# Performance work log

Measured on AMD Instinct MI355X. Metric: run time of the kernel, lower is better.

The kernel has to match this reference:

```python
import jax, jax.numpy as jnp
from jax import lax
import numpy as np

B, P, S, K = 16, 4096, 1024, 16   # clouds, points/cloud, fps samples/cloud (ratio 0.25), knn k
IN_F, OUT_F = 256, 512
EPS = 1e-5


def setup_inputs() -> dict:
    key = jax.random.key(0)
    k1, k2, k3 = jax.random.split(key, 3)
    features = jax.random.normal(k1, (B * P, IN_F), jnp.float32)
    positions = jax.random.normal(k2, (B * P, 3), jnp.float32)
    batch = jnp.repeat(jnp.arange(B, dtype=jnp.int32), P)
    W = jax.random.normal(k3, (IN_F, OUT_F), jnp.float32) / np.sqrt(IN_F)
    b = jnp.zeros((OUT_F,), jnp.float32)
    gamma = jnp.ones((OUT_F,), jnp.float32)
    beta = jnp.zeros((OUT_F,), jnp.float32)
    return {"features": features, "positions": positions, "batch": batch,
            "W": W, "b": b, "gamma": gamma, "beta": beta}


def _fps_local(pos):
    """Farthest point sampling on one cloud. pos: [P,3] -> [S] int32 local indices.
    Deterministic start at index 0 (torch_cluster fps with random_start disabled)."""
    def step(carry, _):
        min_d, last = carry
        d = jnp.sum((pos - pos[last]) ** 2, axis=-1)
        min_d = jnp.minimum(min_d, d)
        nxt = jnp.argmax(min_d).astype(jnp.int32)
        return (min_d, nxt), last
    init = (jnp.full((pos.shape[0],), jnp.inf, pos.dtype), jnp.int32(0))
    _, idx = lax.scan(step, init, None, length=S)
    return idx


def _knn_local(q, x):
    """K nearest neighbors of queries q [S,F] among x [P,F] (squared L2). -> [S,K] int32."""
    d = jnp.sum(q * q, -1, keepdims=True) - 2.0 * (q @ x.T) + jnp.sum(x * x, -1)
    _, idx = lax.top_k(-d, K)
    return idx


def reference(features, positions, batch, W, b, gamma, beta):
    pos_b = positions.reshape(B, P, 3)
    feat_b = features.reshape(B, P, IN_F)

    # --- FPS on positions, per cloud ---
    fps_loc = jax.vmap(_fps_local)(pos_b)                      # [B,S]
    offsets = (jnp.arange(B, dtype=jnp.int32) * P)[:, None]    # [B,1]
    fps_glob = (fps_loc + offsets).reshape(-1)                 # [B*S]

    # --- MLP: Linear -> BatchNorm1d (training batch stats, biased var) -> ReLU ---
    h = features @ W + b                                       # [N,OUT_F]
    mu = jnp.mean(h, axis=0)
    var = jnp.var(h, axis=0)
    h = jax.nn.relu(gamma * (h - mu) * lax.rsqrt(var + EPS) + beta)

    # --- brute-force KNN in feature space: queries = features[fps_indices] ---
    q = jnp.take_along_axis(feat_b, fps_loc[..., None], axis=1)   # [B,S,IN_F]
    nn_loc = jax.vmap(_knn_local)(q, feat_b)                      # [B,S,K]
    nn_glob = nn_loc + offsets[..., None]                         # [B,S,K]

    # --- scatter max-pool: each query has exactly K neighbors -> max over K ---
    nb = h[nn_glob.reshape(-1)].reshape(B, S, K, OUT_F)
    new_features = jnp.max(nb, axis=2).reshape(B * S, OUT_F)

    return new_features, positions[fps_glob], batch[fps_glob]
```

## Files before the change

kernel.cpp:

```cpp
#include <hip/hip_runtime.h>
#include <cstddef>


#define TD_B   16
#define TD_P   4096
#define TD_S   1024
#define TD_K   16
#define TD_INF 256
#define TD_OUTF 512

typedef __attribute__((ext_vector_type(8))) _Float16 half8;
typedef __attribute__((ext_vector_type(4))) float    f32x4;
typedef __attribute__((ext_vector_type(2))) float    v2f;

__device__ __forceinline__ unsigned short f2bf(float x) {
    unsigned u = __float_as_uint(x);
    unsigned r = (u + 0x7fffu + ((u >> 16) & 1u)) >> 16;
    return (unsigned short)r;
}

__device__ __forceinline__ int ld_acq(const int* p) {
    return __hip_atomic_load(p, __ATOMIC_ACQUIRE, __HIP_MEMORY_SCOPE_AGENT);
}
__device__ __forceinline__ void st_rel(int* p, int v) {
    __hip_atomic_store(p, v, __ATOMIC_RELEASE, __HIP_MEMORY_SCOPE_AGENT);
}
__device__ __forceinline__ void add_rel(int* p, int v) {
    __hip_atomic_fetch_add(p, v, __ATOMIC_RELEASE, __HIP_MEMORY_SCOPE_AGENT);
}

struct FpsSm {
    float4 p4[TD_P];
    int    sel[TD_S];
    unsigned long long kw[2][4];
};
struct GemmSm {
    float As[16 * 260];
    float Bs[16 * 128];
};
struct KnnSm {
    union {
        _Float16 x[2][32][264];
        float    dt[256][33];
    } u;
    float QQs[256];
    int   QR[256];
    float xxs[32];
};
struct MergeSm {
    float ld[64][130];
    int   li[64][130];
};
struct MaxpSm { int nbr[128]; };
union SmU {
    FpsSm f; GemmSm g; KnnSm k; MergeSm m; MaxpSm mp;
    char pad_[84000];
};

#define TD_DPPSTEPD(kd_, ctl, bc)                                                       \
    {                                                                                   \
        long long ki_ = __double_as_longlong(kd_);                                      \
        unsigned yh_ = (unsigned)__builtin_amdgcn_update_dpp(                           \
            0, (int)((unsigned long long)ki_ >> 32), (ctl), 0xf, 0xf, (bc));            \
        unsigned yl_ = (unsigned)__builtin_amdgcn_update_dpp(                           \
            0, (int)(unsigned)(unsigned long long)ki_, (ctl), 0xf, 0xf, (bc));          \
        kd_ = fmax(kd_, __hiloint2double((int)yh_, (int)yl_));                          \
    }

__global__ __launch_bounds__(512)
void td_all(const float* __restrict__ feat, const float* __restrict__ pos,
            const float* __restrict__ W, const float* __restrict__ bias,
            const float* __restrict__ gamma, const float* __restrict__ beta,
            unsigned short* __restrict__ H, int* __restrict__ FPSI,
            int* __restrict__ NN, float* __restrict__ P1, float* __restrict__ P2,
            float* __restrict__ SS, float* __restrict__ PD, int* __restrict__ PI,
            float* __restrict__ outF, float* __restrict__ outP,
            float* __restrict__ outB, int* __restrict__ flags) {
    __shared__ SmU sm;
    const int bx = blockIdx.x;
    const int t  = threadIdx.x;

    if (bx < 16) {
        __builtin_amdgcn_s_setprio(2);
        const int b = bx;
        const int w = t >> 6;
        v2f px[8], py[8], pz[8], md[8];
        int ni0[8], ni1[8];
        float lx = 0.0f, ly = 0.0f, lz = 0.0f;
        if (t < 256) {
#pragma unroll
            for (int j = 0; j < 8; ++j) {
                int p0 = j * 512 + t, p1 = p0 + 256;
                const float* q0 = pos + (size_t)(b * TD_P + p0) * 3;
                const float* q1 = pos + (size_t)(b * TD_P + p1) * 3;
                float x0 = q0[0], y0 = q0[1], z0 = q0[2];
                float x1 = q1[0], y1 = q1[1], z1 = q1[2];
                px[j] = (v2f){x0, x1}; py[j] = (v2f){y0, y1}; pz[j] = (v2f){z0, z1};
                sm.f.p4[p0] = make_float4(x0, y0, z0, 0.0f);
                sm.f.p4[p1] = make_float4(x1, y1, z1, 0.0f);
                md[j] = (v2f){__builtin_inff(), __builtin_inff()};
                ni0[j] = ~p0; ni1[j] = ~p1;
            }
            if (t == 0) sm.f.sel[0] = 0;
        }
        __syncthreads();
        if (t < 256) { float4 wp = sm.f.p4[0]; lx = wp.x; ly = wp.y; lz = wp.z; }
        for (int s = 0; s < TD_S - 1; ++s) {
            const int par = s & 1;
            if (t < 256) {
                double k[16];
                {
#pragma clang fp contract(off)
                    v2f l2x = (v2f){lx, lx}, l2y = (v2f){ly, ly}, l2z = (v2f){lz, lz};
#pragma unroll
                    for (int j = 0; j < 8; ++j) {
                        v2f dx = px[j] - l2x;
                        v2f dy = py[j] - l2y;
                        v2f dz = pz[j] - l2z;
                        v2f sx = dx * dx;
                        v2f sy = dy * dy;
                        v2f sz = dz * dz;
                        v2f dd = (sx + sy) + sz;
                        md[j] = __builtin_elementwise_min(md[j], dd);
                        k[2 * j]     = __hiloint2double(__float_as_int(md[j].x), ni0[j]);
                        k[2 * j + 1] = __hiloint2double(__float_as_int(md[j].y), ni1[j]);
                    }
                }
#pragma unroll
                for (int st = 8; st > 0; st >>= 1)
#pragma unroll
                    for (int i = 0; i < st; ++i) k[i] = fmax(k[i], k[i + st]);
                double tk = k[0];
                TD_DPPSTEPD(tk, 0x111, true)
                TD_DPPSTEPD(tk, 0x112, true)
                TD_DPPSTEPD(tk, 0x114, true)
                TD_DPPSTEPD(tk, 0x118, true)
                TD_DPPSTEPD(tk, 0x142, false)
                TD_DPPSTEPD(tk, 0x143, false)
                if ((t & 63) == 63)
                    sm.f.kw[par][w] = (unsigned long long)__double_as_longlong(tk);
            }
            __syncthreads();
            if (t < 256) {
                const double2* kd = (const double2*)sm.f.kw[par];
                double2 va = kd[0], vb = kd[1];
                double gk = fmax(fmax(va.x, va.y), fmax(vb.x, vb.y));
                unsigned idx = ~(unsigned)__double2loint(gk);
                if (t == 0) sm.f.sel[s + 1] = (int)idx;
                float4 wp = sm.f.p4[idx];
                lx = wp.x; ly = wp.y; lz = wp.z;
            }
            if (t < 64 && (s & 127) == 127 && s < 896) {
                int c = s >> 7;
                int i0 = c * 128 + 2 * t;
                FPSI[b * TD_S + i0]     = b * TD_P + sm.f.sel[i0];
                FPSI[b * TD_S + i0 + 1] = b * TD_P + sm.f.sel[i0 + 1];
                __threadfence();
                if (t == 0) st_rel(flags + b, c + 1);
            }
        }
        __syncthreads();
        for (int s = t; s < TD_S; s += 512) {
            int li = sm.f.sel[s];
            int og = b * TD_S + s;
            float4 wp = sm.f.p4[li];
            outP[og * 3 + 0] = wp.x;
            outP[og * 3 + 1] = wp.y;
            outP[og * 3 + 2] = wp.z;
            outB[og] = (float)b;
            FPSI[og] = b * TD_P + li;
        }
        __syncthreads();
        if (t == 0) { __threadfence(); st_rel(flags + b, 8); }
    } else if (bx < 16 + 1024) {
        const int gb = bx - 16;
        const int mb = gb >> 2, nb = gb & 3;
        const int tm = t >> 4, tn = t & 15;
        float acc[8][8];
#pragma unroll
        for (int i = 0; i < 8; ++i)
#pragma unroll
            for (int j = 0; j < 8; ++j) acc[i][j] = 0.0f;
        float* As = sm.g.As;
        float* Bs = sm.g.Bs;
        for (int kc = 0; kc < 16; ++kc) {
#pragma unroll
            for (int p2 = 0; p2 < 2; ++p2) {
                int f4 = t + 512 * p2;
                int r = f4 >> 2, c4 = f4 & 3;
                float4 v = *(const float4*)&feat[(size_t)(mb * 256 + r) * 256 + kc * 16 + c4 * 4];
                As[(c4 * 4 + 0) * 260 + r] = v.x;
                As[(c4 * 4 + 1) * 260 + r] = v.y;
                As[(c4 * 4 + 2) * 260 + r] = v.z;
                As[(c4 * 4 + 3) * 260 + r] = v.w;
            }
            {
                int kk = t >> 5, n4 = t & 31;
                float4 v = *(const float4*)&W[(size_t)(kc * 16 + kk) * 512 + nb * 128 + n4 * 4];
                *(float4*)&Bs[kk * 128 + n4 * 4] = v;
            }
            __syncthreads();
#pragma unroll
            for (int kk = 0; kk < 16; ++kk) {
                float4 a0 = *(float4*)&As[kk * 260 + tm * 8];
                float4 a1 = *(float4*)&As[kk * 260 + tm * 8 + 4];
                float4 b0 = *(float4*)&Bs[kk * 128 + tn * 8];
                float4 b1 = *(float4*)&Bs[kk * 128 + tn * 8 + 4];
                float av[8] = {a0.x, a0.y, a0.z, a0.w, a1.x, a1.y, a1.z, a1.w};
                float bv2[8] = {b0.x, b0.y, b0.z, b0.w, b1.x, b1.y, b1.z, b1.w};
#pragma unroll
                for (int i = 0; i < 8; ++i)
#pragma unroll
                    for (int j = 0; j < 8; ++j)
                        acc[i][j] = fmaf(av[i], bv2[j], acc[i][j]);
            }
            __syncthreads();
        }
        float4 bb0 = *(const float4*)&bias[nb * 128 + tn * 8];
        float4 bb1 = *(const float4*)&bias[nb * 128 + tn * 8 + 4];
        float bsv[8] = {bb0.x, bb0.y, bb0.z, bb0.w, bb1.x, bb1.y, bb1.z, bb1.w};
#pragma unroll
        for (int i = 0; i < 8; ++i) {
            int row = mb * 256 + tm * 8 + i;
            uint4 pk;
            pk.x = (unsigned)f2bf(acc[i][0] + bsv[0]) | ((unsigned)f2bf(acc[i][1] + bsv[1]) << 16);
            pk.y = (unsigned)f2bf(acc[i][2] + bsv[2]) | ((unsigned)f2bf(acc[i][3] + bsv[3]) << 16);
            pk.z = (unsigned)f2bf(acc[i][4] + bsv[4]) | ((unsigned)f2bf(acc[i][5] + bsv[5]) << 16);
            pk.w = (unsigned)f2bf(acc[i][6] + bsv[6]) | ((unsigned)f2bf(acc[i][7] + bsv[7]) << 16);
            *(uint4*)&H[(size_t)row * 512 + nb * 128 + tn * 8] = pk;
        }
        __syncthreads();
        if (t == 0) { __threadfence(); add_rel(flags + 16, 1); }
    } else if (bx < 1552) {
        const int kb = bx - 1040;
        const int b = kb & 15, r2 = kb >> 4;
        const int qqp = r2 >> 3, seg = r2 & 7;
        const int segbase = b * TD_P + seg * 512;
        const int qbase = b * TD_S + qqp * 256;
        if (t == 0) {
            while (ld_acq(flags + b) < 2 * qqp + 2) __builtin_amdgcn_s_sleep(16);
        }
        __syncthreads();
        if (t < 256) sm.k.QR[t] = FPSI[qbase + t];
        __syncthreads();

        const int w = t >> 6, lane = t & 63;
        const int m = lane & 15, quad = lane >> 4;

        half8 qh[2][8], ql[2][8];
#pragma unroll
        for (int qs = 0; qs < 2; ++qs) {
            const float* qp = feat + (size_t)sm.k.QR[w * 32 + qs * 16 + m] * 256;
            float qq2 = 0.0f;
#pragma unroll
            for (int ks = 0; ks < 8; ++ks) {
                float4 f0 = *(const float4*)(qp + ks * 32 + quad * 8);
                float4 f1 = *(const float4*)(qp + ks * 32 + quad * 8 + 4);
                float fv[8] = {f0.x, f0.y, f0.z, f0.w, f1.x, f1.y, f1.z, f1.w};
                half8 h, l;
#pragma unroll
                for (int j = 0; j < 8; ++j) {
                    _Float16 hv = (_Float16)fv[j];
                    h[j] = hv;
                    l[j] = (_Float16)(fv[j] - (float)hv);
                    qq2 = fmaf(fv[j], fv[j], qq2);
                }
                qh[qs][ks] = h; ql[qs][ks] = l;
            }
            qq2 += __shfl_xor(qq2, 16, 64);
            qq2 += __shfl_xor(qq2, 32, 64);
            if (quad == 0) sm.k.QQs[w * 32 + qs * 16 + m] = qq2;
        }

        float sd[16]; int si[16];
#pragma unroll
        for (int r = 0; r < 16; ++r) { sd[r] = __builtin_inff(); si[r] = 0x7fffffff; }

        const int xrow = t >> 4, part = t & 15;

        for (int ct = 0; ct < 16; ++ct) {
            __syncthreads();
            {
                const float* xp = feat + (size_t)(segbase + ct * 32 + xrow) * 256 + part * 16;
                float4 f0 = *(const float4*)(xp);
                float4 f1 = *(const float4*)(xp + 4);
                float4 f2 = *(const float4*)(xp + 8);
                float4 f3 = *(const float4*)(xp + 12);
                float fv[16] = {f0.x, f0.y, f0.z, f0.w, f1.x, f1.y, f1.z, f1.w,
                                f2.x, f2.y, f2.z, f2.w, f3.x, f3.y, f3.z, f3.w};
                half8 h0, h1, l0, l1;
                float cn = 0.0f;
#pragma unroll
                for (int j = 0; j < 8; ++j) {
                    _Float16 hv = (_Float16)fv[j];
                    h0[j] = hv; l0[j] = (_Float16)(fv[j] - (float)hv);
                    cn = fmaf(fv[j], fv[j], cn);
                }
#pragma unroll
                for (int j = 0; j < 8; ++j) {
                    float v = fv[8 + j];
                    _Float16 hv = (_Float16)v;
                    h1[j] = hv; l1[j] = (_Float16)(v - (float)hv);
                    cn = fmaf(v, v, cn);
                }
                *(half8*)&sm.k.u.x[0][xrow][part * 16]     = h0;
                *(half8*)&sm.k.u.x[0][xrow][part * 16 + 8] = h1;
                *(half8*)&sm.k.u.x[1][xrow][part * 16]     = l0;
                *(half8*)&sm.k.u.x[1][xrow][part * 16 + 8] = l1;
                cn += __shfl_xor(cn, 1, 64);
                cn += __shfl_xor(cn, 2, 64);
                cn += __shfl_xor(cn, 4, 64);
                cn += __shfl_xor(cn, 8, 64);
                if (part == 0) sm.k.xxs[xrow] = cn;
            }
            __syncthreads();
            f32x4 acc[2][2];
            acc[0][0] = (f32x4)0.0f; acc[0][1] = (f32x4)0.0f;
            acc[1][0] = (f32x4)0.0f; acc[1][1] = (f32x4)0.0f;
#pragma unroll
            for (int ks = 0; ks < 8; ++ks) {
                half8 xh0 = *(half8*)&sm.k.u.x[0][m][ks * 32 + quad * 8];
                half8 xl0 = *(half8*)&sm.k.u.x[1][m][ks * 32 + quad * 8];
                half8 xh1 = *(half8*)&sm.k.u.x[0][16 + m][ks * 32 + quad * 8];
                half8 xl1 = *(half8*)&sm.k.u.x[1][16 + m][ks * 32 + quad * 8];
                acc[0][0] = __builtin_amdgcn_mfma_f32_16x16x32_f16(ql[0][ks], xh0, acc[0][0], 0, 0, 0);
                acc[0][1] = __builtin_amdgcn_mfma_f32_16x16x32_f16(ql[0][ks], xh1, acc[0][1], 0, 0, 0);
                acc[1][0] = __builtin_amdgcn_mfma_f32_16x16x32_f16(ql[1][ks], xh0, acc[1][0], 0, 0, 0);
                acc[1][1] = __builtin_amdgcn_mfma_f32_16x16x32_f16(ql[1][ks], xh1, acc[1][1], 0, 0, 0);
                acc[0][0] = __builtin_amdgcn_mfma_f32_16x16x32_f16(qh[0][ks], xl0, acc[0][0], 0, 0, 0);
                acc[0][1] = __builtin_amdgcn_mfma_f32_16x16x32_f16(qh[0][ks], xl1, acc[0][1], 0, 0, 0);
                acc[1][0] = __builtin_amdgcn_mfma_f32_16x16x32_f16(qh[1][ks], xl0, acc[1][0], 0, 0, 0);
                acc[1][1] = __builtin_amdgcn_mfma_f32_16x16x32_f16(qh[1][ks], xl1, acc[1][1], 0, 0, 0);
                acc[0][0] = __builtin_amdgcn_mfma_f32_16x16x32_f16(qh[0][ks], xh0, acc[0][0], 0, 0, 0);
                acc[0][1] = __builtin_amdgcn_mfma_f32_16x16x32_f16(qh[0][ks], xh1, acc[0][1], 0, 0, 0);
                acc[1][0] = __builtin_amdgcn_mfma_f32_16x16x32_f16(qh[1][ks], xh0, acc[1][0], 0, 0, 0);
                acc[1][1] = __builtin_amdgcn_mfma_f32_16x16x32_f16(qh[1][ks], xh1, acc[1][1], 0, 0, 0);
            }
            __syncthreads();
            {
                float xx0 = sm.k.xxs[m];
                float xx1 = sm.k.xxs[16 + m];
#pragma unroll
                for (int qs = 0; qs < 2; ++qs) {
                    int qb = w * 32 + qs * 16 + quad * 4;
#pragma unroll
                    for (int reg = 0; reg < 4; ++reg) {
                        float qq = sm.k.QQs[qb + reg];
                        sm.k.u.dt[qb + reg][m]      = (qq - 2.0f * acc[qs][0][reg]) + xx0;
                        sm.k.u.dt[qb + reg][16 + m] = (qq - 2.0f * acc[qs][1][reg]) + xx1;
                    }
                }
            }
            __syncthreads();
            if (t < 256) {
                const int ibase = segbase + ct * 32;
                for (int j = 0; j < 32; ++j) {
                    float d = sm.k.u.dt[t][j];
                    if (d < sd[15]) {
                        sd[15] = d; si[15] = ibase + j;
#pragma unroll
                        for (int r = 15; r > 0; --r) {
                            if (sd[r] < sd[r - 1]) {
                                float td2 = sd[r]; sd[r] = sd[r - 1]; sd[r - 1] = td2;
                                int ti = si[r]; si[r] = si[r - 1]; si[r - 1] = ti;
                            }
                        }
                    }
                }
            }
        }
        if (t < 256) {
            size_t o = ((size_t)(qbase + t)) * 128 + seg * 16;
#pragma unroll
            for (int r = 0; r < 16; ++r) { PD[o + r] = sd[r]; PI[o + r] = si[r]; }
        }
        __syncthreads();
        if (t == 0) { __threadfence(); add_rel(flags + 24 + b * 4 + qqp, 1); }
    } else if (bx < 1808) {
        const int rb = bx - 1552;
        if (t == 0) {
            while (ld_acq(flags + 16) < 1024) __builtin_amdgcn_s_sleep(32);
        }
        __syncthreads();
        if (t < 256) {
            float s1a = 0, s2a = 0, s1b = 0, s2b = 0;
            for (int r = 0; r < 256; ++r) {
                const unsigned* hp = (const unsigned*)(H + (size_t)(rb * 256 + r) * 512);
                unsigned u = hp[t];
                float lo = __uint_as_float(u << 16);
                float hi = __uint_as_float(u & 0xffff0000u);
                s1a += lo; s2a = fmaf(lo, lo, s2a);
                s1b += hi; s2b = fmaf(hi, hi, s2b);
            }
            P1[rb * 512 + 2 * t] = s1a; P1[rb * 512 + 2 * t + 1] = s1b;
            P2[rb * 512 + 2 * t] = s2a; P2[rb * 512 + 2 * t + 1] = s2b;
        }
        __syncthreads();
        if (t == 0) { __threadfence(); add_rel(flags + 17, 1); }
    } else if (bx == 1808) {
        if (t == 0) {
            while (ld_acq(flags + 17) < 256) __builtin_amdgcn_s_sleep(32);
        }
        __syncthreads();
        {
            const int ch = t;
            float s1 = 0, s2 = 0;
            for (int rb2 = 0; rb2 < 256; ++rb2) {
                s1 += P1[rb2 * 512 + ch]; s2 += P2[rb2 * 512 + ch];
            }
            const float invN = 1.0f / 65536.0f;
            float mu  = s1 * invN;
            float var = s2 * invN - mu * mu;
            float sc  = gamma[ch] * (1.0f / sqrtf(var + 1e-5f));
            float sh  = beta[ch] - mu * sc;
            SS[ch] = sc; SS[512 + ch] = sh;
        }
        __syncthreads();
        if (t == 0) { __threadfence(); st_rel(flags + 18, 1); }
    } else if (bx < 2065) {
        const int mb = bx - 1809;
        const int cloud = mb >> 4, qqp = (mb >> 2) & 3;
        if (t == 0) {
            while (ld_acq(flags + 24 + cloud * 4 + qqp) < 8) __builtin_amdgcn_s_sleep(16);
        }
        __syncthreads();
        for (int i = t; i < 64 * 128; i += 512) {
            int qi = i >> 7, j = i & 127;
            sm.m.ld[qi][j] = PD[(size_t)mb * 8192 + i];
            sm.m.li[qi][j] = PI[(size_t)mb * 8192 + i];
        }
        __syncthreads();
        if (t < 64) {
            float sd[16]; int si[16];
#pragma unroll
            for (int r = 0; r < 16; ++r) { sd[r] = __builtin_inff(); si[r] = 0x7fffffff; }
            for (int j = 0; j < 128; ++j) {
                float d = sm.m.ld[t][j];
                if (d < sd[15]) {
                    sd[15] = d; si[15] = sm.m.li[t][j];
#pragma unroll
                    for (int r = 15; r > 0; --r) {
                        if (sd[r] < sd[r - 1]) {
                            float td2 = sd[r]; sd[r] = sd[r - 1]; sd[r - 1] = td2;
                            int ti = si[r]; si[r] = si[r - 1]; si[r - 1] = ti;
                        }
                    }
                }
            }
            int og = (mb * 64 + t) * TD_K;
#pragma unroll
            for (int r = 0; r < 16; ++r) NN[og + r] = si[r];
        }
        __syncthreads();
        if (t == 0) { __threadfence(); st_rel(flags + 96 + mb, 1); }
    } else {
        const int pb = bx - 2065;
        const int qbase8 = pb * 8;
        const int mrg = qbase8 >> 6;
        if (t == 0) {
            while (ld_acq(flags + 96 + mrg) == 0) __builtin_amdgcn_s_sleep(16);
            while (ld_acq(flags + 18) == 0) __builtin_amdgcn_s_sleep(16);
        }
        __syncthreads();
        if (t < 128) sm.mp.nbr[t] = NN[(size_t)qbase8 * 16 + t];
        __syncthreads();
        const int hq = t >> 8, tc = t & 255;
        float sc0 = SS[2 * tc], sc1 = SS[2 * tc + 1];
        float sh0 = SS[512 + 2 * tc], sh1 = SS[512 + 2 * tc + 1];
#pragma unroll
        for (int qi = 0; qi < 4; ++qi) {
            const int q = hq * 4 + qi;
            float m0 = 0.0f, m1 = 0.0f;
#pragma unroll
            for (int k = 0; k < 16; ++k) {
                int row = sm.mp.nbr[q * 16 + k];
                unsigned u = ((const unsigned*)(H + (size_t)row * 512))[tc];
                float lo = __uint_as_float(u << 16);
                float hi = __uint_as_float(u & 0xffff0000u);
                m0 = fmaxf(m0, fmaf(sc0, lo, sh0));
                m1 = fmaxf(m1, fmaf(sc1, hi, sh1));
            }
            float2 o; o.x = m0; o.y = m1;
            *(float2*)&outF[(size_t)(qbase8 + q) * 512 + 2 * tc] = o;
        }
    }
}

extern "C" void kernel_launch(void* const* d_in, const int* in_sizes, int n_in,
                              void* d_out, int out_size, void* d_ws, size_t ws_size,
                              hipStream_t stream) {
    const float* feat  = (const float*)d_in[0];
    const float* pos   = (const float*)d_in[1];
    const float* W     = (const float*)d_in[3];
    const float* bias  = (const float*)d_in[4];
    const float* gamma = (const float*)d_in[5];
    const float* beta  = (const float*)d_in[6];

    char* ws = (char*)d_ws;
    int* flags        = (int*)ws;
    unsigned short* H = (unsigned short*)(ws + 4096);
    int*   FPSI = (int*)  (ws + 67112960);
    int*   NN   = (int*)  (ws + 67178496);
    float* P1   = (float*)(ws + 68227072);
    float* P2   = (float*)(ws + 68751360);
    float* SS   = (float*)(ws + 69275648);
    float* PD   = (float*)(ws + 69279744);
    int*   PI   = (int*)  (ws + 77668352);

    float* outF = (float*)d_out;
    float* outP = outF + (size_t)TD_B * TD_S * TD_OUTF;
    float* outB = outP + (size_t)TD_B * TD_S * 3;

    hipMemsetAsync(flags, 0, 2048, stream);
    td_all<<<4113, 512, 0, stream>>>(feat, pos, W, bias, gamma, beta,
                                     H, FPSI, NN, P1, P2, SS, PD, PI,
                                     outF, outP, outB, flags);
}
```

Measured before the change: 1.181 ms.

## Refine KNN granularity to 128-query chunks and reorder persistent block schedule

The KNN blocks now handle 128 queries per chunk instead of 256, so they can start as soon as each eighth of the FPS samples is ready. Merge and maxpool blocks are regrouped per cloud at finer granularity with new flag indices. The BN stats blocks move ahead of the KNN blocks. The last FPS chunk's blocks are placed at the end of the grid. Shared memory padding is dropped and launch bounds request 4 blocks per CU, aiming for higher occupancy and better overlap with the serial FPS. The cost is more blocks, more flag polling, and extra register pressure under the tighter launch bound.

After: 1.683 ms. 1.43x slower.

```diff
diff --git a/kernel.cpp b/kernel.cpp
--- a/kernel.cpp
+++ b/kernel.cpp
@@ -41,20 +41,19 @@
 struct KnnSm {
     union {
         _Float16 x[2][32][264];
-        float    dt[256][33];
+        float    dt[128][33];
     } u;
-    float QQs[256];
-    int   QR[256];
+    float QQs[128];
+    int   QR[128];
     float xxs[32];
 };
 struct MergeSm {
-    float ld[64][130];
-    int   li[64][130];
+    float ld[32][130];
+    int   li[32][130];
 };
 struct MaxpSm { int nbr[128]; };
 union SmU {
     FpsSm f; GemmSm g; KnnSm k; MergeSm m; MaxpSm mp;
-    char pad_[84000];
 };
 
 #define TD_DPPSTEPD(kd_, ctl, bc)                                                       \
@@ -67,7 +66,7 @@
         kd_ = fmax(kd_, __hiloint2double((int)yh_, (int)yl_));                          \
     }
 
-__global__ __launch_bounds__(512)
+__global__ __launch_bounds__(512, 4)
 void td_all(const float* __restrict__ feat, const float* __restrict__ pos,
             const float* __restrict__ W, const float* __restrict__ bias,
             const float* __restrict__ gamma, const float* __restrict__ beta,
@@ -172,7 +171,7 @@
         }
         __syncthreads();
         if (t == 0) { __threadfence(); st_rel(flags + b, 8); }
-    } else if (bx < 16 + 1024) {
+    } else if (bx < 1040) {
         const int gb = bx - 16;
         const int mb = gb >> 2, nb = gb & 3;
         const int tm = t >> 4, tn = t & 15;
@@ -231,26 +230,67 @@
         }
         __syncthreads();
         if (t == 0) { __threadfence(); add_rel(flags + 16, 1); }
-    } else if (bx < 1552) {
-        const int kb = bx - 1040;
-        const int b = kb & 15, r2 = kb >> 4;
-        const int qqp = r2 >> 3, seg = r2 & 7;
+    } else if (bx < 1296) {
+        const int rb = bx - 1040;
+        if (t == 0) {
+            while (ld_acq(flags + 16) < 1024) __builtin_amdgcn_s_sleep(32);
+        }
+        __syncthreads();
+        if (t < 256) {
+            float s1a = 0, s2a = 0, s1b = 0, s2b = 0;
+            for (int r = 0; r < 256; ++r) {
+                const unsigned* hp = (const unsigned*)(H + (size_t)(rb * 256 + r) * 512);
+                unsigned u = hp[t];
+                float lo = __uint_as_float(u << 16);
+                float hi = __uint_as_float(u & 0xffff0000u);
+                s1a += lo; s2a = fmaf(lo, lo, s2a);
+                s1b += hi; s2b = fmaf(hi, hi, s2b);
+            }
+            P1[rb * 512 + 2 * t] = s1a; P1[rb * 512 + 2 * t + 1] = s1b;
+            P2[rb * 512 + 2 * t] = s2a; P2[rb * 512 + 2 * t + 1] = s2b;
+        }
+        __syncthreads();
+        if (t == 0) { __threadfence(); add_rel(flags + 17, 1); }
+    } else if (bx == 1296) {
+        if (t == 0) {
+            while (ld_acq(flags + 17) < 256) __builtin_amdgcn_s_sleep(32);
+        }
+        __syncthreads();
+        {
+            const int ch = t;
+            float s1 = 0, s2 = 0;
+            for (int rb2 = 0; rb2 < 256; ++rb2) {
+                s1 += P1[rb2 * 512 + ch]; s2 += P2[rb2 * 512 + ch];
+            }
+            const float invN = 1.0f / 65536.0f;
+            float mu  = s1 * invN;
+            float var = s2 * invN - mu * mu;
+            float sc  = gamma[ch] * (1.0f / sqrtf(var + 1e-5f));
+            float sh  = beta[ch] - mu * sc;
+            SS[ch] = sc; SS[512 + ch] = sh;
+        }
+        __syncthreads();
+        if (t == 0) { __threadfence(); st_rel(flags + 18, 1); }
+    } else if (bx < 2193 || (bx >= 4433 && bx < 4561)) {
+        int c, r;
+        if (bx < 2193) { int kb = bx - 1297; c = kb >> 7; r = kb & 127; }
+        else           { r = bx - 4433; c = 7; }
+        const int b = r & 15, seg = r >> 4;
+        const int qbase = b * TD_S + c * 128;
         const int segbase = b * TD_P + seg * 512;
-        const int qbase = b * TD_S + qqp * 256;
         if (t == 0) {
-            while (ld_acq(flags + b) < 2 * qqp + 2) __builtin_amdgcn_s_sleep(16);
-        }
-        __syncthreads();
-        if (t < 256) sm.k.QR[t] = FPSI[qbase + t];
+            while (ld_acq(flags + b) < c + 1) __builtin_amdgcn_s_sleep(16);
+        }
+        __syncthreads();
+        if (t < 128) sm.k.QR[t] = FPSI[qbase + t];
         __syncthreads();
 
         const int w = t >> 6, lane = t & 63;
         const int m = lane & 15, quad = lane >> 4;
 
-        half8 qh[2][8], ql[2][8];
-#pragma unroll
-        for (int qs = 0; qs < 2; ++qs) {
-            const float* qp = feat + (size_t)sm.k.QR[w * 32 + qs * 16 + m] * 256;
+        half8 qh[8], ql[8];
+        {
+            const float* qp = feat + (size_t)sm.k.QR[w * 16 + m] * 256;
             float qq2 = 0.0f;
 #pragma unroll
             for (int ks = 0; ks < 8; ++ks) {
@@ -265,16 +305,16 @@
                     l[j] = (_Float16)(fv[j] - (float)hv);
                     qq2 = fmaf(fv[j], fv[j], qq2);
                 }
-                qh[qs][ks] = h; ql[qs][ks] = l;
+                qh[ks] = h; ql[ks] = l;
             }
             qq2 += __shfl_xor(qq2, 16, 64);
             qq2 += __shfl_xor(qq2, 32, 64);
-            if (quad == 0) sm.k.QQs[w * 32 + qs * 16 + m] = qq2;
+            if (quad == 0) sm.k.QQs[w * 16 + m] = qq2;
         }
 
         float sd[16]; int si[16];
 #pragma unroll
-        for (int r = 0; r < 16; ++r) { sd[r] = __builtin_inff(); si[r] = 0x7fffffff; }
+        for (int rr = 0; rr < 16; ++rr) { sd[rr] = __builtin_inff(); si[rr] = 0x7fffffff; }
 
         const int xrow = t >> 4, part = t & 15;
 
@@ -314,151 +354,119 @@
                 if (part == 0) sm.k.xxs[xrow] = cn;
             }
             __syncthreads();
-            f32x4 acc[2][2];
-            acc[0][0] = (f32x4)0.0f; acc[0][1] = (f32x4)0.0f;
-            acc[1][0] = (f32x4)0.0f; acc[1][1] = (f32x4)0.0f;
-#pragma unroll
-            for (int ks = 0; ks < 8; ++ks) {
-                half8 xh0 = *(half8*)&sm.k.u.x[0][m][ks * 32 + quad * 8];
-                half8 xl0 = *(half8*)&sm.k.u.x[1][m][ks * 32 + quad * 8];
-                half8 xh1 = *(half8*)&sm.k.u.x[0][16 + m][ks * 32 + quad * 8];
-                half8 xl1 = *(half8*)&sm.k.u.x[1][16 + m][ks * 32 + quad * 8];
-                acc[0][0] = __builtin_amdgcn_mfma_f32_16x16x32_f16(ql[0][ks], xh0, acc[0][0], 0, 0, 0);
-                acc[0][1] = __builtin_amdgcn_mfma_f32_16x16x32_f16(ql[0][ks], xh1, acc[0][1], 0, 0, 0);
-                acc[1][0] = __builtin_amdgcn_mfma_f32_16x16x32_f16(ql[1][ks], xh0, acc[1][0], 0, 0, 0);
-                acc[1][1] = __builtin_amdgcn_mfma_f32_16x16x32_f16(ql[1][ks], xh1, acc[1][1], 0, 0, 0);
-                acc[0][0] = __builtin_amdgcn_mfma_f32_16x16x32_f16(qh[0][ks], xl0, acc[0][0], 0, 0, 0);
-                acc[0][1] = __builtin_amdgcn_mfma_f32_16x16x32_f16(qh[0][ks], xl1, acc[0][1], 0, 0, 0);
-                acc[1][0] = __builtin_amdgcn_mfma_f32_16x16x32_f16(qh[1][ks], xl0, acc[1][0], 0, 0, 0);
-                acc[1][1] = __builtin_amdgcn_mfma_f32_16x16x32_f16(qh[1][ks], xl1, acc[1][1], 0, 0, 0);
-                acc[0][0] = __builtin_amdgcn_mfma_f32_16x16x32_f16(qh[0][ks], xh0, acc[0][0], 0, 0, 0);
-                acc[0][1] = __builtin_amdgcn_mfma_f32_16x16x32_f16(qh[0][ks], xh1, acc[0][1], 0, 0, 0);
-                acc[1][0] = __builtin_amdgcn_mfma_f32_16x16x32_f16(qh[1][ks], xh0, acc[1][0], 0, 0, 0);
-                acc[1][1] = __builtin_amdgcn_mfma_f32_16x16x32_f16(qh[1][ks], xh1, acc[1][1], 0, 0, 0);
+            f32x4 a00 = (f32x4)0.0f, a01 = (f32x4)0.0f;
+            f32x4 a10 = (f32x4)0.0f, a11 = (f32x4)0.0f;
+#pragma unroll
+            for (int k2 = 0; k2 < 4; ++k2) {
+                const int ka = 2 * k2, kb2 = 2 * k2 + 1;
+                half8 xh0a = *(half8*)&sm.k.u.x[0][m][ka * 32 + quad * 8];
+                half8 xl0a = *(half8*)&sm.k.u.x[1][m][ka * 32 + quad * 8];
+                half8 xh1a = *(half8*)&sm.k.u.x[0][16 + m][ka * 32 + quad * 8];
+                half8 xl1a = *(half8*)&sm.k.u.x[1][16 + m][ka * 32 + quad * 8];
+                half8 xh0b = *(half8*)&sm.k.u.x[0][m][kb2 * 32 + quad * 8];
+                half8 xl0b = *(half8*)&sm.k.u.x[1][m][kb2 * 32 + quad * 8];
+                half8 xh1b = *(half8*)&sm.k.u.x[0][16 + m][kb2 * 32 + quad * 8];
+                half8 xl1b = *(half8*)&sm.k.u.x[1][16 + m][kb2 * 32 + quad * 8];
+                a00 = __builtin_amdgcn_mfma_f32_16x16x32_f16(ql[ka],  xh0a, a00, 0, 0, 0);
+                a10 = __builtin_amdgcn_mfma_f32_16x16x32_f16(ql[ka],  xh1a, a10, 0, 0, 0);
+                a01 = __builtin_amdgcn_mfma_f32_16x16x32_f16(ql[kb2], xh0b, a01, 0, 0, 0);
+                a11 = __builtin_amdgcn_mfma_f32_16x16x32_f16(ql[kb2], xh1b, a11, 0, 0, 0);
+                a00 = __builtin_amdgcn_mfma_f32_16x16x32_f16(qh[ka],  xl0a, a00, 0, 0, 0);
+                a10 = __builtin_amdgcn_mfma_f32_16x16x32_f16(qh[ka],  xl1a, a10, 0, 0, 0);
+                a01 = __builtin_amdgcn_mfma_f32_16x16x32_f16(qh[kb2], xl0b, a01, 0, 0, 0);
+                a11 = __builtin_amdgcn_mfma_f32_16x16x32_f16(qh[kb2], xl1b, a11, 0, 0, 0);
+                a00 = __builtin_amdgcn_mfma_f32_16x16x32_f16(qh[ka],  xh0a, a00, 0, 0, 0);
+                a10 = __builtin_amdgcn_mfma_f32_16x16x32_f16(qh[ka],  xh1a, a10, 0, 0, 0);
+                a01 = __builtin_amdgcn_mfma_f32_16x16x32_f16(qh[kb2], xh0b, a01, 0, 0, 0);
+                a11 = __builtin_amdgcn_mfma_f32_16x16x32_f16(qh[kb2], xh1b, a11, 0, 0, 0);
             }
             __syncthreads();
             {
                 float xx0 = sm.k.xxs[m];
                 float xx1 = sm.k.xxs[16 + m];
-#pragma unroll
-                for (int qs = 0; qs < 2; ++qs) {
-                    int qb = w * 32 + qs * 16 + quad * 4;
-#pragma unroll
-                    for (int reg = 0; reg < 4; ++reg) {
-                        float qq = sm.k.QQs[qb + reg];
-                        sm.k.u.dt[qb + reg][m]      = (qq - 2.0f * acc[qs][0][reg]) + xx0;
-                        sm.k.u.dt[qb + reg][16 + m] = (qq - 2.0f * acc[qs][1][reg]) + xx1;
-                    }
-                }
-            }
-            __syncthreads();
-            if (t < 256) {
+                int qb = w * 16 + quad * 4;
+#pragma unroll
+                for (int reg = 0; reg < 4; ++reg) {
+                    float qq = sm.k.QQs[qb + reg];
+                    float S0 = a00[reg] + a01[reg];
+                    float S1 = a10[reg] + a11[reg];
+                    sm.k.u.dt[qb + reg][m]      = (qq - 2.0f * S0) + xx0;
+                    sm.k.u.dt[qb + reg][16 + m] = (qq - 2.0f * S1) + xx1;
+                }
+            }
+            __syncthreads();
+            if (t < 128) {
                 const int ibase = segbase + ct * 32;
                 for (int j = 0; j < 32; ++j) {
                     float d = sm.k.u.dt[t][j];
                     if (d < sd[15]) {
                         sd[15] = d; si[15] = ibase + j;
 #pragma unroll
-                        for (int r = 15; r > 0; --r) {
-                            if (sd[r] < sd[r - 1]) {
-                                float td2 = sd[r]; sd[r] = sd[r - 1]; sd[r - 1] = td2;
-                                int ti = si[r]; si[r] = si[r - 1]; si[r - 1] = ti;
+                        for (int rr = 15; rr > 0; --rr) {
+                            if (sd[rr] < sd[rr - 1]) {
+                                float td2 = sd[rr]; sd[rr] = sd[rr - 1]; sd[rr - 1] = td2;
+                                int ti = si[rr]; si[rr] = si[rr - 1]; si[rr - 1] = ti;
                             }
                         }
                     }
                 }
             }
         }
-        if (t < 256) {
+        if (t < 128) {
             size_t o = ((size_t)(qbase + t)) * 128 + seg * 16;
 #pragma unroll
-            for (int r = 0; r < 16; ++r) { PD[o + r] = sd[r]; PI[o + r] = si[r]; }
-        }
-        __syncthreads();
-        if (t == 0) { __threadfence(); add_rel(flags + 24 + b * 4 + qqp, 1); }
-    } else if (bx < 1808) {
-        const int rb = bx - 1552;
+            for (int rr = 0; rr < 16; ++rr) { PD[o + rr] = sd[rr]; PI[o + rr] = si[rr]; }
+        }
+        __syncthreads();
+        if (t == 0) { __threadfence(); add_rel(flags + 32 + b * 8 + c, 1); }
+    } else if (bx < 2641 || (bx >= 4561 && bx < 4625)) {
+        int mb, g;
+        if (bx < 2641) { mb = bx - 2193; g = mb >> 4; }
+        else           { mb = bx - 4561; g = 28 + (mb >> 4); }
+        const int b = mb & 15;
+        const int qg = b * TD_S + g * 32;
         if (t == 0) {
-            while (ld_acq(flags + 16) < 1024) __builtin_amdgcn_s_sleep(32);
-        }
-        __syncthreads();
-        if (t < 256) {
-            float s1a = 0, s2a = 0, s1b = 0, s2b = 0;
-            for (int r = 0; r < 256; ++r) {
-                const unsigned* hp = (const unsigned*)(H + (size_t)(rb * 256 + r) * 512);
-                unsigned u = hp[t];
-                float lo = __uint_as_float(u << 16);
-                float hi = __uint_as_float(u & 0xffff0000u);
-                s1a += lo; s2a = fmaf(lo, lo, s2a);
-                s1b += hi; s2b = fmaf(hi, hi, s2b);
-            }
-            P1[rb * 512 + 2 * t] = s1a; P1[rb * 512 + 2 * t + 1] = s1b;
-            P2[rb * 512 + 2 * t] = s2a; P2[rb * 512 + 2 * t + 1] = s2b;
-        }
-        __syncthreads();
-        if (t == 0) { __threadfence(); add_rel(flags + 17, 1); }
-    } else if (bx == 1808) {
-        if (t == 0) {
-            while (ld_acq(flags + 17) < 256) __builtin_amdgcn_s_sleep(32);
-        }
-        __syncthreads();
-        {
-            const int ch = t;
-            float s1 = 0, s2 = 0;
-            for (int rb2 = 0; rb2 < 256; ++rb2) {
-                s1 += P1[rb2 * 512 + ch]; s2 += P2[rb2 * 512 + ch];
-            }
-            const float invN = 1.0f / 65536.0f;
-            float mu  = s1 * invN;
-            float var = s2 * invN - mu * mu;
-            float sc  = gamma[ch] * (1.0f / sqrtf(var + 1e-5f));
-            float sh  = beta[ch] - mu * sc;
-            SS[ch] = sc; SS[512 + ch] = sh;
-        }
-        __syncthreads();
-        if (t == 0) { __threadfence(); st_rel(flags + 18, 1); }
-    } else if (bx < 2065) {
-        const int mb = bx - 1809;
-        const int cloud = mb >> 4, qqp = (mb >> 2) & 3;
-        if (t == 0) {
-            while (ld_acq(flags + 24 + cloud * 4 + qqp) < 8) __builtin_amdgcn_s_sleep(16);
-        }
-        __syncthreads();
-        for (int i = t; i < 64 * 128; i += 512) {
+            while (ld_acq(flags + 32 + b * 8 + (g >> 2)) < 8) __builtin_amdgcn_s_sleep(16);
+        }
+        __syncthreads();
+        for (int i = t; i < 32 * 128; i += 512) {
             int qi = i >> 7, j = i & 127;
-            sm.m.ld[qi][j] = PD[(size_t)mb * 8192 + i];
-            sm.m.li[qi][j] = PI[(size_t)mb * 8192 + i];
-        }
-        __syncthreads();
-        if (t < 64) {
+            sm.m.ld[qi][j] = PD[(size_t)qg * 128 + i];
+            sm.m.li[qi][j] = PI[(size_t)qg * 128 + i];
+        }
+        __syncthreads();
+        if (t < 32) {
             float sd[16]; int si[16];
 #pragma unroll
-            for (int r = 0; r < 16; ++r) { sd[r] = __builtin_inff(); si[r] = 0x7fffffff; }
+            for (int rr = 0; rr < 16; ++rr) { sd[rr] = __builtin_inff(); si[rr] = 0x7fffffff; }
             for (int j = 0; j < 128; ++j) {
                 float d = sm.m.ld[t][j];
                 if (d < sd[15]) {
                     sd[15] = d; si[15] = sm.m.li[t][j];
 #pragma unroll
-                    for (int r = 15; r > 0; --r) {
-                        if (sd[r] < sd[r - 1]) {
-                            float td2 = sd[r]; sd[r] = sd[r - 1]; sd[r - 1] = td2;
-                            int ti = si[r]; si[r] = si[r - 1]; si[r - 1] = ti;
+                    for (int rr = 15; rr > 0; --rr) {
+                        if (sd[rr] < sd[rr - 1]) {
+                            float td2 = sd[rr]; sd[rr] = sd[rr - 1]; sd[rr - 1] = td2;
+                            int ti = si[rr]; si[rr] = si[rr - 1]; si[rr - 1] = ti;
                         }
                     }
                 }
             }
-            int og = (mb * 64 + t) * TD_K;
-#pragma unroll
-            for (int r = 0; r < 16; ++r) NN[og + r] = si[r];
-        }
-        __syncthreads();
-        if (t == 0) { __threadfence(); st_rel(flags + 96 + mb, 1); }
+            int og = (qg + t) * TD_K;
+#pragma unroll
+            for (int rr = 0; rr < 16; ++rr) NN[og + rr] = si[rr];
+        }
+        __syncthreads();
+        if (t == 0) { __threadfence(); st_rel(flags + 192 + b * 32 + g, 1); }
     } else {
-        const int pb = bx - 2065;
-        const int qbase8 = pb * 8;
-        const int mrg = qbase8 >> 6;
+        int pb, k;
+        if (bx < 4433) { pb = bx - 2641; k = pb >> 4; }
+        else           { pb = bx - 4625; k = 112 + (pb >> 4); }
+        const int b = pb & 15;
+        const int qbase8 = b * TD_S + k * 8;
+        const int g = k >> 2;
         if (t == 0) {
-            while (ld_acq(flags + 96 + mrg) == 0) __builtin_amdgcn_s_sleep(16);
+            while (ld_acq(flags + 192 + b * 32 + g) == 0) __builtin_amdgcn_s_sleep(16);
             while (ld_acq(flags + 18) == 0) __builtin_amdgcn_s_sleep(16);
         }
         __syncthreads();
@@ -472,8 +480,8 @@
             const int q = hq * 4 + qi;
             float m0 = 0.0f, m1 = 0.0f;
 #pragma unroll
-            for (int k = 0; k < 16; ++k) {
-                int row = sm.mp.nbr[q * 16 + k];
+            for (int kk = 0; kk < 16; ++kk) {
+                int row = sm.mp.nbr[q * 16 + kk];
                 unsigned u = ((const unsigned*)(H + (size_t)row * 512))[tc];
                 float lo = __uint_as_float(u << 16);
                 float hi = __uint_as_float(u & 0xffff0000u);
@@ -511,8 +519,8 @@
     float* outP = outF + (size_t)TD_B * TD_S * TD_OUTF;
     float* outB = outP + (size_t)TD_B * TD_S * 3;
 
-    hipMemsetAsync(flags, 0, 2048, stream);
-    td_all<<<4113, 512, 0, stream>>>(feat, pos, W, bias, gamma, beta,
+    hipMemsetAsync(flags, 0, 4096, stream);
+    td_all<<<4881, 512, 0, stream>>>(feat, pos, W, bias, gamma, beta,
                                      H, FPSI, NN, P1, P2, SS, PD, PI,
                                      outF, outP, outB, flags);
 }
```

## Reorder persistent-kernel stages so BN stats precede KNN and tail work interleaves

Applied to the files above, without the earlier changes.

Block ranges in the fused persistent kernel are reordered so the BatchNorm statistics blocks run right after the GEMM and before KNN. KNN, merge and max-pool blocks are re-indexed per cloud and per query chunk. The last FPS chunk's KNN, merge and pool blocks are moved to the end of the grid so earlier chunks can proceed while FPS finishes. Merge blocks now handle 32 queries each, with finer-grained flags, so max-pool can start sooner. The shared-memory pad is removed, which likely raises occupancy, but the grid and flag count grow and there are more spin-waits.

After: 1.369 ms. 1.16x slower.

```diff
diff --git a/kernel.cpp b/kernel.cpp
--- a/kernel.cpp
+++ b/kernel.cpp
@@ -48,13 +48,12 @@
     float xxs[32];
 };
 struct MergeSm {
-    float ld[64][130];
-    int   li[64][130];
+    float ld[32][130];
+    int   li[32][130];
 };
 struct MaxpSm { int nbr[128]; };
 union SmU {
     FpsSm f; GemmSm g; KnnSm k; MergeSm m; MaxpSm mp;
-    char pad_[84000];
 };
 
 #define TD_DPPSTEPD(kd_, ctl, bc)                                                       \
@@ -172,7 +171,7 @@
         }
         __syncthreads();
         if (t == 0) { __threadfence(); st_rel(flags + b, 8); }
-    } else if (bx < 16 + 1024) {
+    } else if (bx < 1040) {
         const int gb = bx - 16;
         const int mb = gb >> 2, nb = gb & 3;
         const int tm = t >> 4, tn = t & 15;
@@ -231,14 +230,56 @@
         }
         __syncthreads();
         if (t == 0) { __threadfence(); add_rel(flags + 16, 1); }
-    } else if (bx < 1552) {
-        const int kb = bx - 1040;
-        const int b = kb & 15, r2 = kb >> 4;
-        const int qqp = r2 >> 3, seg = r2 & 7;
+    } else if (bx < 1296) {
+        const int rb = bx - 1040;
+        if (t == 0) {
+            while (ld_acq(flags + 16) < 1024) __builtin_amdgcn_s_sleep(32);
+        }
+        __syncthreads();
+        if (t < 256) {
+            float s1a = 0, s2a = 0, s1b = 0, s2b = 0;
+            for (int r = 0; r < 256; ++r) {
+                const unsigned* hp = (const unsigned*)(H + (size_t)(rb * 256 + r) * 512);
+                unsigned u = hp[t];
+                float lo = __uint_as_float(u << 16);
+                float hi = __uint_as_float(u & 0xffff0000u);
+                s1a += lo; s2a = fmaf(lo, lo, s2a);
+                s1b += hi; s2b = fmaf(hi, hi, s2b);
+            }
+            P1[rb * 512 + 2 * t] = s1a; P1[rb * 512 + 2 * t + 1] = s1b;
+            P2[rb * 512 + 2 * t] = s2a; P2[rb * 512 + 2 * t + 1] = s2b;
+        }
+        __syncthreads();
+        if (t == 0) { __threadfence(); add_rel(flags + 17, 1); }
+    } else if (bx == 1296) {
+        if (t == 0) {
+            while (ld_acq(flags + 17) < 256) __builtin_amdgcn_s_sleep(32);
+        }
+        __syncthreads();
+        {
+            const int ch = t;
+            float s1 = 0, s2 = 0;
+            for (int rb2 = 0; rb2 < 256; ++rb2) {
+                s1 += P1[rb2 * 512 + ch]; s2 += P2[rb2 * 512 + ch];
+            }
+            const float invN = 1.0f / 65536.0f;
+            float mu  = s1 * invN;
+            float var = s2 * invN - mu * mu;
+            float sc  = gamma[ch] * (1.0f / sqrtf(var + 1e-5f));
+            float sh  = beta[ch] - mu * sc;
+            SS[ch] = sc; SS[512 + ch] = sh;
+        }
+        __syncthreads();
+        if (t == 0) { __threadfence(); st_rel(flags + 18, 1); }
+    } else if (bx < 1681 || (bx >= 3601 && bx < 3729)) {
+        int c, r;
+        if (bx < 1681) { int kb = bx - 1297; c = kb >> 7; r = kb & 127; }
+        else           { r = bx - 3601; c = 3; }
+        const int b = r & 15, seg = r >> 4;
+        const int qbase = b * TD_S + c * 256;
         const int segbase = b * TD_P + seg * 512;
-        const int qbase = b * TD_S + qqp * 256;
         if (t == 0) {
-            while (ld_acq(flags + b) < 2 * qqp + 2) __builtin_amdgcn_s_sleep(16);
+            while (ld_acq(flags + b) < 2 * c + 2) __builtin_amdgcn_s_sleep(16);
         }
         __syncthreads();
         if (t < 256) sm.k.QR[t] = FPSI[qbase + t];
@@ -274,7 +315,7 @@
 
         float sd[16]; int si[16];
 #pragma unroll
-        for (int r = 0; r < 16; ++r) { sd[r] = __builtin_inff(); si[r] = 0x7fffffff; }
+        for (int rr = 0; rr < 16; ++rr) { sd[rr] = __builtin_inff(); si[rr] = 0x7fffffff; }
 
         const int xrow = t >> 4, part = t & 15;
 
@@ -359,10 +400,10 @@
                     if (d < sd[15]) {
                         sd[15] = d; si[15] = ibase + j;
 #pragma unroll
-                        for (int r = 15; r > 0; --r) {
-                            if (sd[r] < sd[r - 1]) {
-                                float td2 = sd[r]; sd[r] = sd[r - 1]; sd[r - 1] = td2;
-                                int ti = si[r]; si[r] = si[r - 1]; si[r - 1] = ti;
+                        for (int rr = 15; rr > 0; --rr) {
+                            if (sd[rr] < sd[rr - 1]) {
+                                float td2 = sd[rr]; sd[rr] = sd[rr - 1]; sd[rr - 1] = td2;
+                                int ti = si[rr]; si[rr] = si[rr - 1]; si[rr - 1] = ti;
                             }
                         }
                     }
@@ -372,93 +413,58 @@
         if (t < 256) {
             size_t o = ((size_t)(qbase + t)) * 128 + seg * 16;
 #pragma unroll
-            for (int r = 0; r < 16; ++r) { PD[o + r] = sd[r]; PI[o + r] = si[r]; }
-        }
-        __syncthreads();
-        if (t == 0) { __threadfence(); add_rel(flags + 24 + b * 4 + qqp, 1); }
-    } else if (bx < 1808) {
-        const int rb = bx - 1552;
+            for (int rr = 0; rr < 16; ++rr) { PD[o + rr] = sd[rr]; PI[o + rr] = si[rr]; }
+        }
+        __syncthreads();
+        if (t == 0) { __threadfence(); add_rel(flags + 32 + b * 4 + c, 1); }
+    } else if (bx < 2065 || (bx >= 3729 && bx < 3857)) {
+        int mb, g;
+        if (bx < 2065) { mb = bx - 1681; g = mb >> 4; }
+        else           { mb = bx - 3729; g = 24 + (mb >> 4); }
+        const int b = mb & 15;
+        const int qg = b * TD_S + g * 32;
         if (t == 0) {
-            while (ld_acq(flags + 16) < 1024) __builtin_amdgcn_s_sleep(32);
-        }
-        __syncthreads();
-        if (t < 256) {
-            float s1a = 0, s2a = 0, s1b = 0, s2b = 0;
-            for (int r = 0; r < 256; ++r) {
-                const unsigned* hp = (const unsigned*)(H + (size_t)(rb * 256 + r) * 512);
-                unsigned u = hp[t];
-                float lo = __uint_as_float(u << 16);
-                float hi = __uint_as_float(u & 0xffff0000u);
-                s1a += lo; s2a = fmaf(lo, lo, s2a);
-                s1b += hi; s2b = fmaf(hi, hi, s2b);
-            }
-            P1[rb * 512 + 2 * t] = s1a; P1[rb * 512 + 2 * t + 1] = s1b;
-            P2[rb * 512 + 2 * t] = s2a; P2[rb * 512 + 2 * t + 1] = s2b;
-        }
-        __syncthreads();
-        if (t == 0) { __threadfence(); add_rel(flags + 17, 1); }
-    } else if (bx == 1808) {
-        if (t == 0) {
-            while (ld_acq(flags + 17) < 256) __builtin_amdgcn_s_sleep(32);
-        }
-        __syncthreads();
-        {
-            const int ch = t;
-            float s1 = 0, s2 = 0;
-            for (int rb2 = 0; rb2 < 256; ++rb2) {
-                s1 += P1[rb2 * 512 + ch]; s2 += P2[rb2 * 512 + ch];
-            }
-            const float invN = 1.0f / 65536.0f;
-            float mu  = s1 * invN;
-            float var = s2 * invN - mu * mu;
-            float sc  = gamma[ch] * (1.0f / sqrtf(var + 1e-5f));
-            float sh  = beta[ch] - mu * sc;
-            SS[ch] = sc; SS[512 + ch] = sh;
-        }
-        __syncthreads();
-        if (t == 0) { __threadfence(); st_rel(flags + 18, 1); }
-    } else if (bx < 2065) {
-        const int mb = bx - 1809;
-        const int cloud = mb >> 4, qqp = (mb >> 2) & 3;
-        if (t == 0) {
-            while (ld_acq(flags + 24 + cloud * 4 + qqp) < 8) __builtin_amdgcn_s_sleep(16);
-        }
-        __syncthreads();
-        for (int i = t; i < 64 * 128; i += 512) {
+            while (ld_acq(flags + 32 + b * 4 + (g >> 3)) < 8) __builtin_amdgcn_s_sleep(16);
+        }
+        __syncthreads();
+        for (int i = t; i < 32 * 128; i += 512) {
             int qi = i >> 7, j = i & 127;
-            sm.m.ld[qi][j] = PD[(size_t)mb * 8192 + i];
-            sm.m.li[qi][j] = PI[(size_t)mb * 8192 + i];
-        }
-        __syncthreads();
-        if (t < 64) {
+            sm.m.ld[qi][j] = PD[(size_t)qg * 128 + i];
+            sm.m.li[qi][j] = PI[(size_t)qg * 128 + i];
+        }
+        __syncthreads();
+        if (t < 32) {
             float sd[16]; int si[16];
 #pragma unroll
-            for (int r = 0; r < 16; ++r) { sd[r] = __builtin_inff(); si[r] = 0x7fffffff; }
+            for (int rr = 0; rr < 16; ++rr) { sd[rr] = __builtin_inff(); si[rr] = 0x7fffffff; }
             for (int j = 0; j < 128; ++j) {
                 float d = sm.m.ld[t][j];
                 if (d < sd[15]) {
                     sd[15] = d; si[15] = sm.m.li[t][j];
 #pragma unroll
-                    for (int r = 15; r > 0; --r) {
-                        if (sd[r] < sd[r - 1]) {
-                            float td2 = sd[r]; sd[r] = sd[r - 1]; sd[r - 1] = td2;
-                            int ti = si[r]; si[r] = si[r - 1]; si[r - 1] = ti;
+                    for (int rr = 15; rr > 0; --rr) {
+                        if (sd[rr] < sd[rr - 1]) {
+                            float td2 = sd[rr]; sd[rr] = sd[rr - 1]; sd[rr - 1] = td2;
+                            int ti = si[rr]; si[rr] = si[rr - 1]; si[rr - 1] = ti;
                         }
                     }
                 }
             }
-            int og = (mb * 64 + t) * TD_K;
-#pragma unroll
-            for (int r = 0; r < 16; ++r) NN[og + r] = si[r];
-        }
-        __syncthreads();
-        if (t == 0) { __threadfence(); st_rel(flags + 96 + mb, 1); }
+            int og = (qg + t) * TD_K;
+#pragma unroll
+            for (int rr = 0; rr < 16; ++rr) NN[og + rr] = si[rr];
+        }
+        __syncthreads();
+        if (t == 0) { __threadfence(); st_rel(flags + 192 + b * 32 + g, 1); }
     } else {
-        const int pb = bx - 2065;
-        const int qbase8 = pb * 8;
-        const int mrg = qbase8 >> 6;
+        int pb, k;
+        if (bx < 3601) { pb = bx - 2065; k = pb >> 4; }
+        else           { pb = bx - 3857; k = 96 + (pb >> 4); }
+        const int b = pb & 15;
+        const int qbase8 = b * TD_S + k * 8;
+        const int g = k >> 2;
         if (t == 0) {
-            while (ld_acq(flags + 96 + mrg) == 0) __builtin_amdgcn_s_sleep(16);
+            while (ld_acq(flags + 192 + b * 32 + g) == 0) __builtin_amdgcn_s_sleep(16);
             while (ld_acq(flags + 18) == 0) __builtin_amdgcn_s_sleep(16);
         }
         __syncthreads();
@@ -472,8 +478,8 @@
             const int q = hq * 4 + qi;
             float m0 = 0.0f, m1 = 0.0f;
 #pragma unroll
-            for (int k = 0; k < 16; ++k) {
-                int row = sm.mp.nbr[q * 16 + k];
+            for (int kk = 0; kk < 16; ++kk) {
+                int row = sm.mp.nbr[q * 16 + kk];
                 unsigned u = ((const unsigned*)(H + (size_t)row * 512))[tc];
                 float lo = __uint_as_float(u << 16);
                 float hi = __uint_as_float(u & 0xffff0000u);
@@ -511,8 +517,8 @@
     float* outP = outF + (size_t)TD_B * TD_S * TD_OUTF;
     float* outB = outP + (size_t)TD_B * TD_S * 3;
 
-    hipMemsetAsync(flags, 0, 2048, stream);
-    td_all<<<4113, 512, 0, stream>>>(feat, pos, W, bias, gamma, beta,
+    hipMemsetAsync(flags, 0, 4096, stream);
+    td_all<<<4369, 512, 0, stream>>>(feat, pos, W, bias, gamma, beta,
                                      H, FPSI, NN, P1, P2, SS, PD, PI,
                                      outF, outP, outB, flags);
 }
```
